# Performance work log

Measured on AMD Instinct MI355X. Metric: run time of the kernel, lower is better.

Reference implementation:

```python
import jax, jax.numpy as jnp
import numpy as np

T, H, I, E = 1024, 2048, 3200, 8  # tokens, hidden, intermediate, experts
JITTER_EPS = 0.01


def sparsemixer(scores, jitter_eps=JITTER_EPS):
    # ---- top-1 ----
    max1 = jnp.max(scores, axis=-1, keepdims=True)
    ind1 = jnp.argmax(scores, axis=-1, keepdims=True)  # first-max, matches torch
    factor = jnp.maximum(jnp.abs(scores), max1)        # clamp(min=max1)
    mask = (max1 - scores) / factor > 2.0 * jitter_eps
    masked_gates = jax.nn.softmax(jnp.where(mask, -jnp.inf, scores), axis=-1)
    mult1 = jnp.take_along_axis(masked_gates, ind1, axis=-1)
    # ---- mask out top-1, then top-2 ----
    top1_onehot = jax.nn.one_hot(ind1[..., 0], scores.shape[-1], dtype=bool)
    masked_scores = jnp.where(top1_onehot, -jnp.inf, scores)
    max2 = jnp.max(masked_scores, axis=-1, keepdims=True)
    ind2 = jnp.argmax(masked_scores, axis=-1, keepdims=True)
    factor2 = jnp.maximum(jnp.abs(scores), max2)
    mask2 = (max2 - scores) / factor2 > 2.0 * jitter_eps
    masked_gates2 = jax.nn.softmax(jnp.where(mask2, -jnp.inf, masked_scores), axis=-1)
    mult2 = jnp.take_along_axis(masked_gates2, ind2, axis=-1)
    multiplier = jnp.concatenate([mult1, mult2], axis=-1)       # [T, 2]
    selected = jnp.concatenate([ind1, ind2], axis=-1)           # [T, 2] int
    return multiplier, selected


def setup_inputs() -> dict:
    key = jax.random.key(0)
    k0, k1, k2, k3, k4 = jax.random.split(key, 5)
    hidden_states = jax.random.normal(k0, (T, H), dtype=jnp.float32)
    gate_w = jax.random.normal(k1, (E, H), dtype=jnp.float32) * (H ** -0.5)
    w1 = jax.random.normal(k2, (E, I, H), dtype=jnp.float32) * (H ** -0.5)
    w3 = jax.random.normal(k3, (E, I, H), dtype=jnp.float32) * (H ** -0.5)
    w2 = jax.random.normal(k4, (E, H, I), dtype=jnp.float32) * (I ** -0.5)
    return {"hidden_states": hidden_states, "gate_w": gate_w,
            "w1": w1, "w3": w3, "w2": w2}


def reference(hidden_states, gate_w, w1, w3, w2):
    x = hidden_states.reshape(-1, gate_w.shape[1])              # [T, H]
    router_logits = x @ gate_w.T                                # [T, E]
    topk_w, topk_ids = sparsemixer(router_logits)               # [T,2], [T,2]
    n_exp = gate_w.shape[0]
    # combine top-2 (weight, id) pairs into a dense [T, E] gate matrix
    gates = jnp.sum(jax.nn.one_hot(topk_ids, n_exp, dtype=x.dtype)
                    * topk_w[..., None], axis=1)                # [T, E]
    # SiLU-gated expert MLPs, combined with routing gates
    h1 = jnp.einsum('th,eih->tei', x, w1)                       # [T, E, I]
    h3 = jnp.einsum('th,eih->tei', x, w3)
    act = jax.nn.silu(h1) * h3                                  # [T, E, I]
    out = jnp.einsum('tei,ehi,te->th', act, w2, gates)          # [T, H]
    return out.reshape(hidden_states.shape)
```

## Files before the change

### kernel.cpp

```cpp
#include <hip/hip_runtime.h>

#define T_ 1024
#define H_ 2048
#define I_ 3200
#define E_ 8

typedef float fvec4 __attribute__((ext_vector_type(4)));
typedef float f32x4 __attribute__((ext_vector_type(4)));
typedef __bf16 bf16x8 __attribute__((ext_vector_type(8)));
typedef unsigned short u16x8 __attribute__((ext_vector_type(8)));
typedef unsigned short u16x4 __attribute__((ext_vector_type(4)));

typedef const __attribute__((address_space(1))) void* gp1_t;
typedef __attribute__((address_space(3))) void* sp3_t;

#define WS_TOK   128
#define WS_GATE  32896
#define WS_XB    65664
#define WS_ACT   4259968

__device__ __forceinline__ unsigned short f2bf(float f) {
  unsigned u = __builtin_bit_cast(unsigned, f);
  u += 0x7FFFu + ((u >> 16) & 1u);
  return (unsigned short)(u >> 16);
}

__global__ __launch_bounds__(256) void cvt_x_kernel(const float* __restrict__ x,
                                                    unsigned short* __restrict__ xb) {
  int i = blockIdx.x * 256 + threadIdx.x;
  fvec4 v = reinterpret_cast<const fvec4*>(x)[i];
  u16x4 o;
  o[0] = f2bf(v[0]); o[1] = f2bf(v[1]); o[2] = f2bf(v[2]); o[3] = f2bf(v[3]);
  reinterpret_cast<u16x4*>(xb)[i] = o;
}

__global__ __launch_bounds__(256) void router_kernel(const float* __restrict__ x,
                                                     const float* __restrict__ gw,
                                                     int* __restrict__ cnt,
                                                     int* __restrict__ tok,
                                                     float* __restrict__ gate) {
  const int lane = threadIdx.x & 63;
  const int wv = threadIdx.x >> 6;
  const int t = blockIdx.x * 4 + wv;

  float xr[32];
  const float* xp = x + (size_t)t * H_;
#pragma unroll
  for (int j = 0; j < 32; j++) xr[j] = xp[j * 64 + lane];

  float s[E_];
#pragma unroll
  for (int e = 0; e < E_; e++) {
    const float* gp = gw + (size_t)e * H_;
    float p = 0.f;
#pragma unroll
    for (int j = 0; j < 32; j++) p = fmaf(xr[j], gp[j * 64 + lane], p);
#pragma unroll
    for (int off = 32; off > 0; off >>= 1) p += __shfl_xor(p, off);
    s[e] = p;
  }

  float max1 = s[0]; int i1 = 0;
#pragma unroll
  for (int e = 1; e < E_; e++) if (s[e] > max1) { max1 = s[e]; i1 = e; }
  float den1 = 0.f;
#pragma unroll
  for (int e = 0; e < E_; e++) {
    float factor = fmaxf(fabsf(s[e]), max1);
    if ((max1 - s[e]) <= 0.02f * factor) den1 += expf(s[e] - max1);
  }
  float mult1 = 1.f / den1;

  float max2 = -INFINITY; int i2 = 0;
#pragma unroll
  for (int e = 0; e < E_; e++) if (e != i1 && s[e] > max2) { max2 = s[e]; i2 = e; }
  float den2 = 0.f;
#pragma unroll
  for (int e = 0; e < E_; e++) {
    if (e == i1) continue;
    float factor = fmaxf(fabsf(s[e]), max2);
    if ((max2 - s[e]) <= 0.02f * factor) den2 += expf(s[e] - max2);
  }
  float mult2 = 1.f / den2;

  if (lane == 0) {
    int p1 = atomicAdd(&cnt[i1], 1); tok[i1 * T_ + p1] = t; gate[i1 * T_ + p1] = mult1;
    int p2 = atomicAdd(&cnt[i2], 1); tok[i2 * T_ + p2] = t; gate[i2 * T_ + p2] = mult2;
  }
}

__global__ void prefix_kernel(const int* __restrict__ cnt, int* __restrict__ base) {
  if (threadIdx.x == 0 && blockIdx.x == 0) {
    int a = 0;
    for (int e = 0; e < E_; e++) { base[e] = a; a += (cnt[e] + 127) & ~127; }
    base[E_] = a;
  }
}

__global__ __launch_bounds__(256, 2) void ffn1_kernel(
    const unsigned short* __restrict__ xb, const float* __restrict__ w1,
    const float* __restrict__ w3, const int* __restrict__ cnt,
    const int* __restrict__ base, const int* __restrict__ tokl,
    unsigned short* __restrict__ actb) {
  const int e = blockIdx.z;
  const int ab = base[e];
  const int padcnt = base[e + 1] - ab;
  const int m_base = blockIdx.y * 256;
  if (m_base >= padcnt) return;
  const int count = cnt[e];
  const int n0 = blockIdx.x * 64;
  const int tid = threadIdx.x;
  const int lane = tid & 63, wv = tid >> 6;
  const int wm = wv >> 1, wn = wv & 1;

  __shared__ unsigned short Ash[2][256 * 64];
  __shared__ unsigned short B1s[64 * 64];
  __shared__ unsigned short B3s[64 * 64];

  const unsigned short* aSrc[8];
  const int colg = ((lane & 7) ^ ((lane >> 3) & 7)) * 8;
#pragma unroll
  for (int i = 0; i < 8; ++i) {
    int r = m_base + wv * 64 + i * 8 + (lane >> 3);
    if (r >= count) r = count - 1;
    aSrc[i] = xb + (size_t)tokl[e * T_ + r] * H_ + colg;
  }
  const int brow = tid >> 2;
  const int bc = (tid & 3) * 16;
  const float* b1p = w1 + ((size_t)e * I_ + n0 + brow) * H_ + bc;
  const float* b3p = w3 + ((size_t)e * I_ + n0 + brow) * H_ + bc;

#pragma unroll
  for (int i = 0; i < 8; ++i) {
    __builtin_amdgcn_global_load_lds((gp1_t)aSrc[i], (sp3_t)&Ash[0][(wv * 64 + i * 8) * 64], 16, 0, 0);
    aSrc[i] += 64;
  }
  fvec4 r1[4], r3[4];
#pragma unroll
  for (int j = 0; j < 4; ++j) { r1[j] = *(const fvec4*)(b1p + j * 4); r3[j] = *(const fvec4*)(b3p + j * 4); }
  b1p += 64; b3p += 64;

  f32x4 acc1[2][4][2], acc3[2][4][2];
#pragma unroll
  for (int mt = 0; mt < 2; ++mt)
#pragma unroll
    for (int mi = 0; mi < 4; ++mi)
#pragma unroll
      for (int ni = 0; ni < 2; ++ni) {
        acc1[mt][mi][ni] = (f32x4){0.f, 0.f, 0.f, 0.f};
        acc3[mt][mi][ni] = (f32x4){0.f, 0.f, 0.f, 0.f};
      }

  const int swz = brow & 7;
  const int c0 = (tid & 3) * 2;
  char* pB1 = (char*)B1s + brow * 128;
  char* pB3 = (char*)B3s + brow * 128;

  for (int t = 0; t < H_ / 64; ++t) {
    const int cur = t & 1;
    asm volatile("s_waitcnt vmcnt(0)" ::: "memory");
#pragma unroll
    for (int c = 0; c < 2; ++c) {
      fvec4 lo = r1[c * 2], hi = r1[c * 2 + 1];
      u16x8 v;
      v[0] = f2bf(lo[0]); v[1] = f2bf(lo[1]); v[2] = f2bf(lo[2]); v[3] = f2bf(lo[3]);
      v[4] = f2bf(hi[0]); v[5] = f2bf(hi[1]); v[6] = f2bf(hi[2]); v[7] = f2bf(hi[3]);
      *(u16x8*)(pB1 + (((c0 + c) ^ swz) << 4)) = v;
      fvec4 lo3 = r3[c * 2], hi3 = r3[c * 2 + 1];
      u16x8 w;
      w[0] = f2bf(lo3[0]); w[1] = f2bf(lo3[1]); w[2] = f2bf(lo3[2]); w[3] = f2bf(lo3[3]);
      w[4] = f2bf(hi3[0]); w[5] = f2bf(hi3[1]); w[6] = f2bf(hi3[2]); w[7] = f2bf(hi3[3]);
      *(u16x8*)(pB3 + (((c0 + c) ^ swz) << 4)) = w;
    }
    __syncthreads();
    if (t + 1 < H_ / 64) {
#pragma unroll
      for (int i = 0; i < 8; ++i) {
        __builtin_amdgcn_global_load_lds((gp1_t)aSrc[i],
            (sp3_t)&Ash[cur ^ 1][(wv * 64 + i * 8) * 64], 16, 0, 0);
        aSrc[i] += 64;
      }
#pragma unroll
      for (int j = 0; j < 4; ++j) { r1[j] = *(const fvec4*)(b1p + j * 4); r3[j] = *(const fvec4*)(b3p + j * 4); }
      b1p += 64; b3p += 64;
    }
    const unsigned short* Ac = Ash[cur];
#pragma unroll
    for (int kk = 0; kk < 2; ++kk) {
      const int c16 = kk * 4 + (lane >> 4);
      bf16x8 b1f[2], b3f[2];
#pragma unroll
      for (int ni = 0; ni < 2; ++ni) {
        int br_ = wn * 32 + ni * 16 + (lane & 15);
        b1f[ni] = *(const bf16x8*)((const char*)B1s + br_ * 128 + ((c16 ^ (br_ & 7)) << 4));
        b3f[ni] = *(const bf16x8*)((const char*)B3s + br_ * 128 + ((c16 ^ (br_ & 7)) << 4));
      }
#pragma unroll
      for (int mt = 0; mt < 2; ++mt) {
        bf16x8 af[4];
#pragma unroll
        for (int mi = 0; mi < 4; ++mi) {
          int ar = mt * 128 + wm * 64 + mi * 16 + (lane & 15);
          af[mi] = *(const bf16x8*)((const char*)Ac + ar * 128 + ((c16 ^ (ar & 7)) << 4));
        }
#pragma unroll
        for (int mi = 0; mi < 4; ++mi)
#pragma unroll
          for (int ni = 0; ni < 2; ++ni) {
            acc1[mt][mi][ni] = __builtin_amdgcn_mfma_f32_16x16x32_bf16(af[mi], b1f[ni], acc1[mt][mi][ni], 0, 0, 0);
            acc3[mt][mi][ni] = __builtin_amdgcn_mfma_f32_16x16x32_bf16(af[mi], b3f[ni], acc3[mt][mi][ni], 0, 0, 0);
          }
      }
    }
    __syncthreads();
  }

  const int row_lim = padcnt - m_base;
#pragma unroll
  for (int mt = 0; mt < 2; ++mt)
#pragma unroll
    for (int mi = 0; mi < 4; ++mi)
#pragma unroll
      for (int ni = 0; ni < 2; ++ni) {
        f32x4 v1 = acc1[mt][mi][ni], v3 = acc3[mt][mi][ni];
#pragma unroll
        for (int j = 0; j < 4; ++j) {
          int row = mt * 128 + wm * 64 + mi * 16 + (lane >> 4) * 4 + j;
          if (row < row_lim) {
            float h1 = v1[j];
            float a = (h1 / (1.f + __expf(-h1))) * v3[j];
            actb[(size_t)(ab + m_base + row) * I_ + n0 + wn * 32 + ni * 16 + (lane & 15)] = f2bf(a);
          }
        }
      }
}

__global__ __launch_bounds__(256, 2) void ffn2_kernel(
    const unsigned short* __restrict__ actb, const float* __restrict__ w2,
    const int* __restrict__ cnt, const int* __restrict__ base,
    const int* __restrict__ tokl, const float* __restrict__ gatel,
    float* __restrict__ out) {
  const int e = blockIdx.z;
  const int count = cnt[e];
  const int m_base = blockIdx.y * 256;
  if (m_base >= count) return;
  const int ab = base[e];
  const int n0 = blockIdx.x * 64;
  const int tid = threadIdx.x;
  const int lane = tid & 63, wv = tid >> 6;
  const int wm = wv >> 1, wn = wv & 1;

  __shared__ unsigned short Ash[2][256 * 64];
  __shared__ unsigned short Bs[64 * 64];
  __shared__ int tokS[256];
  __shared__ float gateS[256];

  if (tid < 256) {
    int r = m_base + tid;
    bool vld = r < count;
    tokS[tid] = vld ? tokl[e * T_ + r] : 0;
    gateS[tid] = vld ? gatel[e * T_ + r] : 0.f;
  }

  const unsigned short* aSrc[8];
  const int colg = ((lane & 7) ^ ((lane >> 3) & 7)) * 8;
#pragma unroll
  for (int i = 0; i < 8; ++i) {
    int r = ab + m_base + wv * 64 + i * 8 + (lane >> 3);
    aSrc[i] = actb + (size_t)r * I_ + colg;
  }
  const int brow = tid >> 2;
  const int bc = (tid & 3) * 16;
  const float* bp = w2 + ((size_t)e * H_ + n0 + brow) * I_ + bc;

#pragma unroll
  for (int i = 0; i < 8; ++i) {
    __builtin_amdgcn_global_load_lds((gp1_t)aSrc[i], (sp3_t)&Ash[0][(wv * 64 + i * 8) * 64], 16, 0, 0);
    aSrc[i] += 64;
  }
  fvec4 r2[4];
#pragma unroll
  for (int j = 0; j < 4; ++j) r2[j] = *(const fvec4*)(bp + j * 4);
  bp += 64;

  f32x4 acc[2][4][2];
#pragma unroll
  for (int mt = 0; mt < 2; ++mt)
#pragma unroll
    for (int mi = 0; mi < 4; ++mi)
#pragma unroll
      for (int ni = 0; ni < 2; ++ni) acc[mt][mi][ni] = (f32x4){0.f, 0.f, 0.f, 0.f};

  const int swz = brow & 7;
  const int c0 = (tid & 3) * 2;
  char* pB = (char*)Bs + brow * 128;

  for (int t = 0; t < I_ / 64; ++t) {
    const int cur = t & 1;
    asm volatile("s_waitcnt vmcnt(0)" ::: "memory");
#pragma unroll
    for (int c = 0; c < 2; ++c) {
      fvec4 lo = r2[c * 2], hi = r2[c * 2 + 1];
      u16x8 v;
      v[0] = f2bf(lo[0]); v[1] = f2bf(lo[1]); v[2] = f2bf(lo[2]); v[3] = f2bf(lo[3]);
      v[4] = f2bf(hi[0]); v[5] = f2bf(hi[1]); v[6] = f2bf(hi[2]); v[7] = f2bf(hi[3]);
      *(u16x8*)(pB + (((c0 + c) ^ swz) << 4)) = v;
    }
    __syncthreads();
    if (t + 1 < I_ / 64) {
#pragma unroll
      for (int i = 0; i < 8; ++i) {
        __builtin_amdgcn_global_load_lds((gp1_t)aSrc[i],
            (sp3_t)&Ash[cur ^ 1][(wv * 64 + i * 8) * 64], 16, 0, 0);
        aSrc[i] += 64;
      }
#pragma unroll
      for (int j = 0; j < 4; ++j) r2[j] = *(const fvec4*)(bp + j * 4);
      bp += 64;
    }
    const unsigned short* Ac = Ash[cur];
#pragma unroll
    for (int kk = 0; kk < 2; ++kk) {
      const int c16 = kk * 4 + (lane >> 4);
      bf16x8 bf[2];
#pragma unroll
      for (int ni = 0; ni < 2; ++ni) {
        int br_ = wn * 32 + ni * 16 + (lane & 15);
        bf[ni] = *(const bf16x8*)((const char*)Bs + br_ * 128 + ((c16 ^ (br_ & 7)) << 4));
      }
#pragma unroll
      for (int mt = 0; mt < 2; ++mt) {
        bf16x8 af[4];
#pragma unroll
        for (int mi = 0; mi < 4; ++mi) {
          int ar = mt * 128 + wm * 64 + mi * 16 + (lane & 15);
          af[mi] = *(const bf16x8*)((const char*)Ac + ar * 128 + ((c16 ^ (ar & 7)) << 4));
        }
#pragma unroll
        for (int mi = 0; mi < 4; ++mi)
#pragma unroll
          for (int ni = 0; ni < 2; ++ni)
            acc[mt][mi][ni] = __builtin_amdgcn_mfma_f32_16x16x32_bf16(af[mi], bf[ni], acc[mt][mi][ni], 0, 0, 0);
      }
    }
    __syncthreads();
  }

#pragma unroll
  for (int mt = 0; mt < 2; ++mt)
#pragma unroll
    for (int mi = 0; mi < 4; ++mi)
#pragma unroll
      for (int ni = 0; ni < 2; ++ni)
#pragma unroll
        for (int j = 0; j < 4; ++j) {
          int row = mt * 128 + wm * 64 + mi * 16 + (lane >> 4) * 4 + j;
          if (m_base + row < count) {
            int col = n0 + wn * 32 + ni * 16 + (lane & 15);
            atomicAdd(&out[(size_t)tokS[row] * H_ + col], gateS[row] * acc[mt][mi][ni][j]);
          }
        }
}

extern "C" void kernel_launch(void* const* d_in, const int* in_sizes, int n_in,
                              void* d_out, int out_size, void* d_ws, size_t ws_size,
                              hipStream_t stream) {
  const float* x  = (const float*)d_in[0];
  const float* gw = (const float*)d_in[1];
  const float* w1 = (const float*)d_in[2];
  const float* w3 = (const float*)d_in[3];
  const float* w2 = (const float*)d_in[4];
  float* out = (float*)d_out;
  char* ws = (char*)d_ws;

  int* cnt = (int*)ws;
  int* base = (int*)(ws + 64);
  int* tokl = (int*)(ws + WS_TOK);
  float* gatel = (float*)(ws + WS_GATE);
  unsigned short* xb = (unsigned short*)(ws + WS_XB);
  unsigned short* actb = (unsigned short*)(ws + WS_ACT);

  (void)hipMemsetAsync(d_out, 0, (size_t)T_ * H_ * sizeof(float), stream);
  (void)hipMemsetAsync(ws, 0, 64, stream);

  cvt_x_kernel<<<(T_ * H_ / 4 + 255) / 256, 256, 0, stream>>>(x, xb);
  router_kernel<<<T_ / 4, 256, 0, stream>>>(x, gw, cnt, tokl, gatel);
  prefix_kernel<<<1, 64, 0, stream>>>(cnt, base);
  ffn1_kernel<<<dim3(I_ / 64, 4, E_), 256, 0, stream>>>(xb, w1, w3, cnt, base, tokl, actb);
  ffn2_kernel<<<dim3(H_ / 64, 4, E_), 256, 0, stream>>>(actb, w2, cnt, base, tokl, gatel, out);
}
```

Baseline: 352.0 us.

## Restructure MoE GEMMs: 512-thread blocks, register-loaded A, double-buffered B, fused x conversion

```diff
diff --git a/kernel.cpp b/kernel.cpp
--- a/kernel.cpp
+++ b/kernel.cpp
@@ -8,53 +8,51 @@
 typedef float fvec4 __attribute__((ext_vector_type(4)));
 typedef float f32x4 __attribute__((ext_vector_type(4)));
 typedef __bf16 bf16x8 __attribute__((ext_vector_type(8)));
-typedef unsigned short u16x8 __attribute__((ext_vector_type(8)));
 typedef unsigned short u16x4 __attribute__((ext_vector_type(4)));
-
-typedef const __attribute__((address_space(1))) void* gp1_t;
-typedef __attribute__((address_space(3))) void* sp3_t;
 
 #define WS_TOK   128
 #define WS_GATE  32896
 #define WS_XB    65664
 #define WS_ACT   4259968
 
-__device__ __forceinline__ unsigned short f2bf(float f) {
-  unsigned u = __builtin_bit_cast(unsigned, f);
-  u += 0x7FFFu + ((u >> 16) & 1u);
-  return (unsigned short)(u >> 16);
-}
-
-__global__ __launch_bounds__(256) void cvt_x_kernel(const float* __restrict__ x,
-                                                    unsigned short* __restrict__ xb) {
-  int i = blockIdx.x * 256 + threadIdx.x;
-  fvec4 v = reinterpret_cast<const fvec4*>(x)[i];
-  u16x4 o;
-  o[0] = f2bf(v[0]); o[1] = f2bf(v[1]); o[2] = f2bf(v[2]); o[3] = f2bf(v[3]);
-  reinterpret_cast<u16x4*>(xb)[i] = o;
-}
+#define BAR() do { asm volatile("s_waitcnt lgkmcnt(0)" ::: "memory"); \
+    __builtin_amdgcn_sched_barrier(0); __builtin_amdgcn_s_barrier(); } while (0)
 
 __global__ __launch_bounds__(256) void router_kernel(const float* __restrict__ x,
                                                      const float* __restrict__ gw,
                                                      int* __restrict__ cnt,
                                                      int* __restrict__ tok,
-                                                     float* __restrict__ gate) {
+                                                     float* __restrict__ gate,
+                                                     unsigned short* __restrict__ xb) {
   const int lane = threadIdx.x & 63;
   const int wv = threadIdx.x >> 6;
   const int t = blockIdx.x * 4 + wv;
 
-  float xr[32];
   const float* xp = x + (size_t)t * H_;
-#pragma unroll
-  for (int j = 0; j < 32; j++) xr[j] = xp[j * 64 + lane];
+  fvec4 xr[8];
+#pragma unroll
+  for (int j = 0; j < 8; ++j) xr[j] = *(const fvec4*)(xp + j * 256 + lane * 4);
+
+  unsigned short* xbp = xb + (size_t)t * H_;
+#pragma unroll
+  for (int j = 0; j < 8; ++j) {
+    u16x4 o;
+#pragma unroll
+    for (int c = 0; c < 4; ++c) o[c] = __builtin_bit_cast(unsigned short, (__bf16)xr[j][c]);
+    *(u16x4*)(xbp + j * 256 + lane * 4) = o;
+  }
 
   float s[E_];
 #pragma unroll
-  for (int e = 0; e < E_; e++) {
+  for (int e = 0; e < E_; ++e) {
     const float* gp = gw + (size_t)e * H_;
     float p = 0.f;
 #pragma unroll
-    for (int j = 0; j < 32; j++) p = fmaf(xr[j], gp[j * 64 + lane], p);
+    for (int j = 0; j < 8; ++j) {
+      fvec4 g = *(const fvec4*)(gp + j * 256 + lane * 4);
+      p = fmaf(xr[j][0], g[0], p); p = fmaf(xr[j][1], g[1], p);
+      p = fmaf(xr[j][2], g[2], p); p = fmaf(xr[j][3], g[3], p);
+    }
 #pragma unroll
     for (int off = 32; off > 0; off >>= 1) p += __shfl_xor(p, off);
     s[e] = p;
@@ -62,10 +60,10 @@
 
   float max1 = s[0]; int i1 = 0;
 #pragma unroll
-  for (int e = 1; e < E_; e++) if (s[e] > max1) { max1 = s[e]; i1 = e; }
+  for (int e = 1; e < E_; ++e) if (s[e] > max1) { max1 = s[e]; i1 = e; }
   float den1 = 0.f;
 #pragma unroll
-  for (int e = 0; e < E_; e++) {
+  for (int e = 0; e < E_; ++e) {
     float factor = fmaxf(fabsf(s[e]), max1);
     if ((max1 - s[e]) <= 0.02f * factor) den1 += expf(s[e] - max1);
   }
@@ -73,10 +71,10 @@
 
   float max2 = -INFINITY; int i2 = 0;
 #pragma unroll
-  for (int e = 0; e < E_; e++) if (e != i1 && s[e] > max2) { max2 = s[e]; i2 = e; }
+  for (int e = 0; e < E_; ++e) if (e != i1 && s[e] > max2) { max2 = s[e]; i2 = e; }
   float den2 = 0.f;
 #pragma unroll
-  for (int e = 0; e < E_; e++) {
+  for (int e = 0; e < E_; ++e) {
     if (e == i1) continue;
     float factor = fmaxf(fabsf(s[e]), max2);
     if ((max2 - s[e]) <= 0.02f * factor) den2 += expf(s[e] - max2);
@@ -92,12 +90,12 @@
 __global__ void prefix_kernel(const int* __restrict__ cnt, int* __restrict__ base) {
   if (threadIdx.x == 0 && blockIdx.x == 0) {
     int a = 0;
-    for (int e = 0; e < E_; e++) { base[e] = a; a += (cnt[e] + 127) & ~127; }
+    for (int e = 0; e < E_; ++e) { base[e] = a; a += (cnt[e] + 127) & ~127; }
     base[E_] = a;
   }
 }
 
-__global__ __launch_bounds__(256, 2) void ffn1_kernel(
+__global__ __launch_bounds__(512, 2) void ffn1_kernel(
     const unsigned short* __restrict__ xb, const float* __restrict__ w1,
     const float* __restrict__ w3, const int* __restrict__ cnt,
     const int* __restrict__ base, const int* __restrict__ tokl,
@@ -113,129 +111,118 @@
   const int lane = tid & 63, wv = tid >> 6;
   const int wm = wv >> 1, wn = wv & 1;
 
-  __shared__ unsigned short Ash[2][256 * 64];
-  __shared__ unsigned short B1s[64 * 64];
-  __shared__ unsigned short B3s[64 * 64];
-
-  const unsigned short* aSrc[8];
-  const int colg = ((lane & 7) ^ ((lane >> 3) & 7)) * 8;
-#pragma unroll
-  for (int i = 0; i < 8; ++i) {
-    int r = m_base + wv * 64 + i * 8 + (lane >> 3);
+  __shared__ unsigned short B1s[2][64 * 64];
+  __shared__ unsigned short B3s[2][64 * 64];
+
+  const unsigned short* aPtr[4];
+#pragma unroll
+  for (int mi = 0; mi < 4; ++mi) {
+    int r = m_base + wm * 64 + mi * 16 + (lane & 15);
     if (r >= count) r = count - 1;
-    aSrc[i] = xb + (size_t)tokl[e * T_ + r] * H_ + colg;
-  }
-  const int brow = tid >> 2;
-  const int bc = (tid & 3) * 16;
-  const float* b1p = w1 + ((size_t)e * I_ + n0 + brow) * H_ + bc;
-  const float* b3p = w3 + ((size_t)e * I_ + n0 + brow) * H_ + bc;
-
-#pragma unroll
-  for (int i = 0; i < 8; ++i) {
-    __builtin_amdgcn_global_load_lds((gp1_t)aSrc[i], (sp3_t)&Ash[0][(wv * 64 + i * 8) * 64], 16, 0, 0);
-    aSrc[i] += 64;
-  }
-  fvec4 r1[4], r3[4];
-#pragma unroll
-  for (int j = 0; j < 4; ++j) { r1[j] = *(const fvec4*)(b1p + j * 4); r3[j] = *(const fvec4*)(b3p + j * 4); }
-  b1p += 64; b3p += 64;
-
-  f32x4 acc1[2][4][2], acc3[2][4][2];
-#pragma unroll
-  for (int mt = 0; mt < 2; ++mt)
-#pragma unroll
-    for (int mi = 0; mi < 4; ++mi)
+    aPtr[mi] = xb + (size_t)tokl[e * T_ + r] * H_ + (lane >> 4) * 8;
+  }
+  const int brow = tid >> 3;
+  const float* b1p = w1 + ((size_t)e * I_ + n0 + brow) * H_ + (tid & 7) * 8;
+  const float* b3p = w3 + ((size_t)e * I_ + n0 + brow) * H_ + (tid & 7) * 8;
+  const int wbyte = brow * 128 + (((tid & 7) ^ (brow & 7)) << 4);
+
+  int rb[2][2];
+#pragma unroll
+  for (int ni = 0; ni < 2; ++ni) {
+    int br_ = wn * 32 + ni * 16 + (lane & 15);
+#pragma unroll
+    for (int kk = 0; kk < 2; ++kk)
+      rb[ni][kk] = br_ * 128 + (((kk * 4 + (lane >> 4)) ^ (br_ & 7)) << 4);
+  }
+
+  f32x4 acc1[4][2], acc3[4][2];
+#pragma unroll
+  for (int mi = 0; mi < 4; ++mi)
+#pragma unroll
+    for (int ni = 0; ni < 2; ++ni) { acc1[mi][ni] = (f32x4){0,0,0,0}; acc3[mi][ni] = (f32x4){0,0,0,0}; }
+
+  bf16x8 aA[4][2], aB[4][2];
+  fvec4 b1e[2], b3e[2], b1o[2], b3o[2];
+
+  auto LOADA = [&](bf16x8 (&as)[4][2], int kb) {
+#pragma unroll
+    for (int mi = 0; mi < 4; ++mi) {
+      as[mi][0] = *(const bf16x8*)(aPtr[mi] + kb);
+      as[mi][1] = *(const bf16x8*)(aPtr[mi] + kb + 32);
+    }
+  };
+  auto LOADB = [&](fvec4 (&r1)[2], fvec4 (&r3)[2], int kb) {
+    r1[0] = *(const fvec4*)(b1p + kb); r1[1] = *(const fvec4*)(b1p + kb + 4);
+    r3[0] = *(const fvec4*)(b3p + kb); r3[1] = *(const fvec4*)(b3p + kb + 4);
+  };
+  auto CVTW = [&](fvec4 (&r1)[2], fvec4 (&r3)[2], int buf) {
+    bf16x8 v, w;
+#pragma unroll
+    for (int c = 0; c < 4; ++c) {
+      v[c] = (__bf16)r1[0][c]; v[c + 4] = (__bf16)r1[1][c];
+      w[c] = (__bf16)r3[0][c]; w[c + 4] = (__bf16)r3[1][c];
+    }
+    *(bf16x8*)((char*)B1s[buf] + wbyte) = v;
+    *(bf16x8*)((char*)B3s[buf] + wbyte) = w;
+  };
+  auto COMPUTE = [&](bf16x8 (&as)[4][2], int buf) {
+    __builtin_amdgcn_s_setprio(1);
+#pragma unroll
+    for (int kk = 0; kk < 2; ++kk) {
+      bf16x8 f1[2], f3[2];
 #pragma unroll
       for (int ni = 0; ni < 2; ++ni) {
-        acc1[mt][mi][ni] = (f32x4){0.f, 0.f, 0.f, 0.f};
-        acc3[mt][mi][ni] = (f32x4){0.f, 0.f, 0.f, 0.f};
+        f1[ni] = *(const bf16x8*)((const char*)B1s[buf] + rb[ni][kk]);
+        f3[ni] = *(const bf16x8*)((const char*)B3s[buf] + rb[ni][kk]);
       }
-
-  const int swz = brow & 7;
-  const int c0 = (tid & 3) * 2;
-  char* pB1 = (char*)B1s + brow * 128;
-  char* pB3 = (char*)B3s + brow * 128;
-
-  for (int t = 0; t < H_ / 64; ++t) {
-    const int cur = t & 1;
-    asm volatile("s_waitcnt vmcnt(0)" ::: "memory");
-#pragma unroll
-    for (int c = 0; c < 2; ++c) {
-      fvec4 lo = r1[c * 2], hi = r1[c * 2 + 1];
-      u16x8 v;
-      v[0] = f2bf(lo[0]); v[1] = f2bf(lo[1]); v[2] = f2bf(lo[2]); v[3] = f2bf(lo[3]);
-      v[4] = f2bf(hi[0]); v[5] = f2bf(hi[1]); v[6] = f2bf(hi[2]); v[7] = f2bf(hi[3]);
-      *(u16x8*)(pB1 + (((c0 + c) ^ swz) << 4)) = v;
-      fvec4 lo3 = r3[c * 2], hi3 = r3[c * 2 + 1];
-      u16x8 w;
-      w[0] = f2bf(lo3[0]); w[1] = f2bf(lo3[1]); w[2] = f2bf(lo3[2]); w[3] = f2bf(lo3[3]);
-      w[4] = f2bf(hi3[0]); w[5] = f2bf(hi3[1]); w[6] = f2bf(hi3[2]); w[7] = f2bf(hi3[3]);
-      *(u16x8*)(pB3 + (((c0 + c) ^ swz) << 4)) = w;
-    }
-    __syncthreads();
-    if (t + 1 < H_ / 64) {
-#pragma unroll
-      for (int i = 0; i < 8; ++i) {
-        __builtin_amdgcn_global_load_lds((gp1_t)aSrc[i],
-            (sp3_t)&Ash[cur ^ 1][(wv * 64 + i * 8) * 64], 16, 0, 0);
-        aSrc[i] += 64;
-      }
-#pragma unroll
-      for (int j = 0; j < 4; ++j) { r1[j] = *(const fvec4*)(b1p + j * 4); r3[j] = *(const fvec4*)(b3p + j * 4); }
-      b1p += 64; b3p += 64;
-    }
-    const unsigned short* Ac = Ash[cur];
-#pragma unroll
-    for (int kk = 0; kk < 2; ++kk) {
-      const int c16 = kk * 4 + (lane >> 4);
-      bf16x8 b1f[2], b3f[2];
-#pragma unroll
-      for (int ni = 0; ni < 2; ++ni) {
-        int br_ = wn * 32 + ni * 16 + (lane & 15);
-        b1f[ni] = *(const bf16x8*)((const char*)B1s + br_ * 128 + ((c16 ^ (br_ & 7)) << 4));
-        b3f[ni] = *(const bf16x8*)((const char*)B3s + br_ * 128 + ((c16 ^ (br_ & 7)) << 4));
-      }
-#pragma unroll
-      for (int mt = 0; mt < 2; ++mt) {
-        bf16x8 af[4];
-#pragma unroll
-        for (int mi = 0; mi < 4; ++mi) {
-          int ar = mt * 128 + wm * 64 + mi * 16 + (lane & 15);
-          af[mi] = *(const bf16x8*)((const char*)Ac + ar * 128 + ((c16 ^ (ar & 7)) << 4));
+#pragma unroll
+      for (int mi = 0; mi < 4; ++mi)
+#pragma unroll
+        for (int ni = 0; ni < 2; ++ni) {
+          acc1[mi][ni] = __builtin_amdgcn_mfma_f32_16x16x32_bf16(as[mi][kk], f1[ni], acc1[mi][ni], 0, 0, 0);
+          acc3[mi][ni] = __builtin_amdgcn_mfma_f32_16x16x32_bf16(as[mi][kk], f3[ni], acc3[mi][ni], 0, 0, 0);
         }
-#pragma unroll
-        for (int mi = 0; mi < 4; ++mi)
-#pragma unroll
-          for (int ni = 0; ni < 2; ++ni) {
-            acc1[mt][mi][ni] = __builtin_amdgcn_mfma_f32_16x16x32_bf16(af[mi], b1f[ni], acc1[mt][mi][ni], 0, 0, 0);
-            acc3[mt][mi][ni] = __builtin_amdgcn_mfma_f32_16x16x32_bf16(af[mi], b3f[ni], acc3[mt][mi][ni], 0, 0, 0);
-          }
-      }
-    }
-    __syncthreads();
+    }
+    __builtin_amdgcn_s_setprio(0);
+  };
+
+  const int NT = H_ / 64;
+  LOADB(b1e, b3e, 0);
+  LOADA(aA, 0);
+  CVTW(b1e, b3e, 0);
+  LOADB(b1o, b3o, 64);
+  BAR();
+  for (int t = 0; t < NT; t += 2) {
+    LOADA(aB, (t + 1) * 64);
+    if (t + 2 < NT) LOADB(b1e, b3e, (t + 2) * 64);
+    COMPUTE(aA, 0);
+    CVTW(b1o, b3o, 1);
+    BAR();
+    if (t + 2 < NT) LOADA(aA, (t + 2) * 64);
+    if (t + 3 < NT) LOADB(b1o, b3o, (t + 3) * 64);
+    COMPUTE(aB, 1);
+    if (t + 2 < NT) CVTW(b1e, b3e, 0);
+    BAR();
   }
 
   const int row_lim = padcnt - m_base;
 #pragma unroll
-  for (int mt = 0; mt < 2; ++mt)
-#pragma unroll
-    for (int mi = 0; mi < 4; ++mi)
-#pragma unroll
-      for (int ni = 0; ni < 2; ++ni) {
-        f32x4 v1 = acc1[mt][mi][ni], v3 = acc3[mt][mi][ni];
-#pragma unroll
-        for (int j = 0; j < 4; ++j) {
-          int row = mt * 128 + wm * 64 + mi * 16 + (lane >> 4) * 4 + j;
-          if (row < row_lim) {
-            float h1 = v1[j];
-            float a = (h1 / (1.f + __expf(-h1))) * v3[j];
-            actb[(size_t)(ab + m_base + row) * I_ + n0 + wn * 32 + ni * 16 + (lane & 15)] = f2bf(a);
-          }
+  for (int mi = 0; mi < 4; ++mi)
+#pragma unroll
+    for (int ni = 0; ni < 2; ++ni)
+#pragma unroll
+      for (int j = 0; j < 4; ++j) {
+        int row = wm * 64 + mi * 16 + (lane >> 4) * 4 + j;
+        if (row < row_lim) {
+          float h1 = acc1[mi][ni][j];
+          float a = (h1 / (1.f + __expf(-h1))) * acc3[mi][ni][j];
+          actb[(size_t)(ab + m_base + row) * I_ + n0 + wn * 32 + ni * 16 + (lane & 15)] =
+              __builtin_bit_cast(unsigned short, (__bf16)a);
         }
       }
 }
 
-__global__ __launch_bounds__(256, 2) void ffn2_kernel(
+__global__ __launch_bounds__(512, 2) void ffn2_kernel(
     const unsigned short* __restrict__ actb, const float* __restrict__ w2,
     const int* __restrict__ cnt, const int* __restrict__ base,
     const int* __restrict__ tokl, const float* __restrict__ gatel,
@@ -250,116 +237,102 @@
   const int lane = tid & 63, wv = tid >> 6;
   const int wm = wv >> 1, wn = wv & 1;
 
-  __shared__ unsigned short Ash[2][256 * 64];
-  __shared__ unsigned short Bs[64 * 64];
-  __shared__ int tokS[256];
-  __shared__ float gateS[256];
-
-  if (tid < 256) {
-    int r = m_base + tid;
-    bool vld = r < count;
-    tokS[tid] = vld ? tokl[e * T_ + r] : 0;
-    gateS[tid] = vld ? gatel[e * T_ + r] : 0.f;
-  }
-
-  const unsigned short* aSrc[8];
-  const int colg = ((lane & 7) ^ ((lane >> 3) & 7)) * 8;
-#pragma unroll
-  for (int i = 0; i < 8; ++i) {
-    int r = ab + m_base + wv * 64 + i * 8 + (lane >> 3);
-    aSrc[i] = actb + (size_t)r * I_ + colg;
-  }
-  const int brow = tid >> 2;
-  const int bc = (tid & 3) * 16;
-  const float* bp = w2 + ((size_t)e * H_ + n0 + brow) * I_ + bc;
-
-#pragma unroll
-  for (int i = 0; i < 8; ++i) {
-    __builtin_amdgcn_global_load_lds((gp1_t)aSrc[i], (sp3_t)&Ash[0][(wv * 64 + i * 8) * 64], 16, 0, 0);
-    aSrc[i] += 64;
-  }
-  fvec4 r2[4];
-#pragma unroll
-  for (int j = 0; j < 4; ++j) r2[j] = *(const fvec4*)(bp + j * 4);
-  bp += 64;
-
-  f32x4 acc[2][4][2];
-#pragma unroll
-  for (int mt = 0; mt < 2; ++mt)
-#pragma unroll
-    for (int mi = 0; mi < 4; ++mi)
-#pragma unroll
-      for (int ni = 0; ni < 2; ++ni) acc[mt][mi][ni] = (f32x4){0.f, 0.f, 0.f, 0.f};
-
-  const int swz = brow & 7;
-  const int c0 = (tid & 3) * 2;
-  char* pB = (char*)Bs + brow * 128;
-
-  for (int t = 0; t < I_ / 64; ++t) {
-    const int cur = t & 1;
-    asm volatile("s_waitcnt vmcnt(0)" ::: "memory");
-#pragma unroll
-    for (int c = 0; c < 2; ++c) {
-      fvec4 lo = r2[c * 2], hi = r2[c * 2 + 1];
-      u16x8 v;
-      v[0] = f2bf(lo[0]); v[1] = f2bf(lo[1]); v[2] = f2bf(lo[2]); v[3] = f2bf(lo[3]);
-      v[4] = f2bf(hi[0]); v[5] = f2bf(hi[1]); v[6] = f2bf(hi[2]); v[7] = f2bf(hi[3]);
-      *(u16x8*)(pB + (((c0 + c) ^ swz) << 4)) = v;
-    }
-    __syncthreads();
-    if (t + 1 < I_ / 64) {
-#pragma unroll
-      for (int i = 0; i < 8; ++i) {
-        __builtin_amdgcn_global_load_lds((gp1_t)aSrc[i],
-            (sp3_t)&Ash[cur ^ 1][(wv * 64 + i * 8) * 64], 16, 0, 0);
-        aSrc[i] += 64;
+  __shared__ unsigned short Bs[2][64 * 64];
+
+  const unsigned short* aPtr[4];
+#pragma unroll
+  for (int mi = 0; mi < 4; ++mi) {
+    int r = ab + m_base + wm * 64 + mi * 16 + (lane & 15);
+    aPtr[mi] = actb + (size_t)r * I_ + (lane >> 4) * 8;
+  }
+  const int brow = tid >> 3;
+  const float* bp = w2 + ((size_t)e * H_ + n0 + brow) * I_ + (tid & 7) * 8;
+  const int wbyte = brow * 128 + (((tid & 7) ^ (brow & 7)) << 4);
+
+  int rb[2][2];
+#pragma unroll
+  for (int ni = 0; ni < 2; ++ni) {
+    int br_ = wn * 32 + ni * 16 + (lane & 15);
+#pragma unroll
+    for (int kk = 0; kk < 2; ++kk)
+      rb[ni][kk] = br_ * 128 + (((kk * 4 + (lane >> 4)) ^ (br_ & 7)) << 4);
+  }
+
+  f32x4 acc[4][2];
+#pragma unroll
+  for (int mi = 0; mi < 4; ++mi)
+#pragma unroll
+    for (int ni = 0; ni < 2; ++ni) acc[mi][ni] = (f32x4){0,0,0,0};
+
+  bf16x8 aA[4][2], aB[4][2];
+  fvec4 be[2], bo[2];
+
+  auto LOADA = [&](bf16x8 (&as)[4][2], int kb) {
+#pragma unroll
+    for (int mi = 0; mi < 4; ++mi) {
+      as[mi][0] = *(const bf16x8*)(aPtr[mi] + kb);
+      as[mi][1] = *(const bf16x8*)(aPtr[mi] + kb + 32);
+    }
+  };
+  auto LOADB = [&](fvec4 (&r)[2], int kb) {
+    r[0] = *(const fvec4*)(bp + kb); r[1] = *(const fvec4*)(bp + kb + 4);
+  };
+  auto CVTW = [&](fvec4 (&r)[2], int buf) {
+    bf16x8 v;
+#pragma unroll
+    for (int c = 0; c < 4; ++c) { v[c] = (__bf16)r[0][c]; v[c + 4] = (__bf16)r[1][c]; }
+    *(bf16x8*)((char*)Bs[buf] + wbyte) = v;
+  };
+  auto COMPUTE = [&](bf16x8 (&as)[4][2], int buf) {
+    __builtin_amdgcn_s_setprio(1);
+#pragma unroll
+    for (int kk = 0; kk < 2; ++kk) {
+      bf16x8 f[2];
+#pragma unroll
+      for (int ni = 0; ni < 2; ++ni)
+        f[ni] = *(const bf16x8*)((const char*)Bs[buf] + rb[ni][kk]);
+#pragma unroll
+      for (int mi = 0; mi < 4; ++mi)
+#pragma unroll
+        for (int ni = 0; ni < 2; ++ni)
+          acc[mi][ni] = __builtin_amdgcn_mfma_f32_16x16x32_bf16(as[mi][kk], f[ni], acc[mi][ni], 0, 0, 0);
+    }
+    __builtin_amdgcn_s_setprio(0);
+  };
+
+  const int NT = I_ / 64;
+  LOADB(be, 0);
+  LOADA(aA, 0);
+  CVTW(be, 0);
+  LOADB(bo, 64);
+  BAR();
+  for (int t = 0; t < NT; t += 2) {
+    LOADA(aB, (t + 1) * 64);
+    if (t + 2 < NT) LOADB(be, (t + 2) * 64);
+    COMPUTE(aA, 0);
+    CVTW(bo, 1);
+    BAR();
+    if (t + 2 < NT) LOADA(aA, (t + 2) * 64);
+    if (t + 3 < NT) LOADB(bo, (t + 3) * 64);
+    COMPUTE(aB, 1);
+    if (t + 2 < NT) CVTW(be, 0);
+    BAR();
+  }
+
+#pragma unroll
+  for (int mi = 0; mi < 4; ++mi)
+#pragma unroll
+    for (int j = 0; j < 4; ++j) {
+      int row = m_base + wm * 64 + mi * 16 + (lane >> 4) * 4 + j;
+      if (row < count) {
+        int tokv = tokl[e * T_ + row];
+        float g = gatel[e * T_ + row];
+#pragma unroll
+        for (int ni = 0; ni < 2; ++ni)
+          atomicAdd(&out[(size_t)tokv * H_ + n0 + wn * 32 + ni * 16 + (lane & 15)],
+                    g * acc[mi][ni][j]);
       }
-#pragma unroll
-      for (int j = 0; j < 4; ++j) r2[j] = *(const fvec4*)(bp + j * 4);
-      bp += 64;
-    }
-    const unsigned short* Ac = Ash[cur];
-#pragma unroll
-    for (int kk = 0; kk < 2; ++kk) {
-      const int c16 = kk * 4 + (lane >> 4);
-      bf16x8 bf[2];
-#pragma unroll
-      for (int ni = 0; ni < 2; ++ni) {
-        int br_ = wn * 32 + ni * 16 + (lane & 15);
-        bf[ni] = *(const bf16x8*)((const char*)Bs + br_ * 128 + ((c16 ^ (br_ & 7)) << 4));
-      }
-#pragma unroll
-      for (int mt = 0; mt < 2; ++mt) {
-        bf16x8 af[4];
-#pragma unroll
-        for (int mi = 0; mi < 4; ++mi) {
-          int ar = mt * 128 + wm * 64 + mi * 16 + (lane & 15);
-          af[mi] = *(const bf16x8*)((const char*)Ac + ar * 128 + ((c16 ^ (ar & 7)) << 4));
-        }
-#pragma unroll
-        for (int mi = 0; mi < 4; ++mi)
-#pragma unroll
-          for (int ni = 0; ni < 2; ++ni)
-            acc[mt][mi][ni] = __builtin_amdgcn_mfma_f32_16x16x32_bf16(af[mi], bf[ni], acc[mt][mi][ni], 0, 0, 0);
-      }
-    }
-    __syncthreads();
-  }
-
-#pragma unroll
-  for (int mt = 0; mt < 2; ++mt)
-#pragma unroll
-    for (int mi = 0; mi < 4; ++mi)
-#pragma unroll
-      for (int ni = 0; ni < 2; ++ni)
-#pragma unroll
-        for (int j = 0; j < 4; ++j) {
-          int row = mt * 128 + wm * 64 + mi * 16 + (lane >> 4) * 4 + j;
-          if (m_base + row < count) {
-            int col = n0 + wn * 32 + ni * 16 + (lane & 15);
-            atomicAdd(&out[(size_t)tokS[row] * H_ + col], gateS[row] * acc[mt][mi][ni][j]);
-          }
-        }
+    }
 }
 
 extern "C" void kernel_launch(void* const* d_in, const int* in_sizes, int n_in,
@@ -383,9 +356,8 @@
   (void)hipMemsetAsync(d_out, 0, (size_t)T_ * H_ * sizeof(float), stream);
   (void)hipMemsetAsync(ws, 0, 64, stream);
 
-  cvt_x_kernel<<<(T_ * H_ / 4 + 255) / 256, 256, 0, stream>>>(x, xb);
-  router_kernel<<<T_ / 4, 256, 0, stream>>>(x, gw, cnt, tokl, gatel);
+  router_kernel<<<T_ / 4, 256, 0, stream>>>(x, gw, cnt, tokl, gatel, xb);
   prefix_kernel<<<1, 64, 0, stream>>>(cnt, base);
-  ffn1_kernel<<<dim3(I_ / 64, 4, E_), 256, 0, stream>>>(xb, w1, w3, cnt, base, tokl, actb);
-  ffn2_kernel<<<dim3(H_ / 64, 4, E_), 256, 0, stream>>>(actb, w2, cnt, base, tokl, gatel, out);
-}
+  ffn1_kernel<<<dim3(I_ / 64, 4, E_), 512, 0, stream>>>(xb, w1, w3, cnt, base, tokl, actb);
+  ffn2_kernel<<<dim3(H_ / 64, 4, E_), 512, 0, stream>>>(actb, w2, cnt, base, tokl, gatel, out);
+}
```

Result: slower. 523.7 us (+48.8%).
